# Performance work log

Measured on AMD Instinct MI355X. Metric: run time of the kernel, lower is better.

Reference implementation:

```python
import jax, jax.numpy as jnp
import numpy as np

H = 64
NUM_HEADS = 4
NUM_LAYERS = 2
B = 524288
EPS = 1e-5


def _layernorm(x, g, b):
    mu = jnp.mean(x, axis=-1, keepdims=True)
    var = jnp.mean((x - mu) ** 2, axis=-1, keepdims=True)
    return (x - mu) * jax.lax.rsqrt(var + EPS) * g + b


def _mha(x, w_qkv, b_qkv, w_o, b_o):
    # x: (B, M, H). Fused in-proj like torch nn.MultiheadAttention.
    Bx, M, Hx = x.shape
    hd = Hx // NUM_HEADS
    qkv = x @ w_qkv.T + b_qkv                      # (B, M, 3H)
    q, k, v = jnp.split(qkv, 3, axis=-1)
    q = q.reshape(Bx, M, NUM_HEADS, hd)
    k = k.reshape(Bx, M, NUM_HEADS, hd)
    v = v.reshape(Bx, M, NUM_HEADS, hd)
    scores = jnp.einsum('bqnd,bknd->bnqk', q, k) / jnp.sqrt(jnp.asarray(hd, x.dtype))
    a = jax.nn.softmax(scores, axis=-1)
    o = jnp.einsum('bnqk,bknd->bqnd', a, v).reshape(Bx, M, Hx)
    return o @ w_o.T + b_o


def _block(x, rel, p):
    attn_out = _mha(x, p['w_qkv'], p['b_qkv'], p['w_o'], p['b_o'])
    attn_out = attn_out * rel[:, :, None]
    x = _layernorm(x + attn_out, p['n1_g'], p['n1_b'])
    ffn = jax.nn.relu(x @ p['ffn_w'].T + p['ffn_b'])
    return _layernorm(x + ffn, p['n2_g'], p['n2_b'])


def setup_inputs() -> dict:
    key = jax.random.key(0)
    ks = jax.random.split(key, 32)
    inp = {
        'h_poi': jax.random.normal(ks[0], (B, H), jnp.float32),
        'h_census': jax.random.normal(ks[1], (B, H), jnp.float32),
        'h_traffic': jax.random.normal(ks[2], (B, H), jnp.float32),
        'mfr_poi': jax.random.uniform(ks[3], (B, 2), jnp.float32),
        'mfr_census': jax.random.uniform(ks[4], (B, 2), jnp.float32),
        'mfr_traffic': jax.random.uniform(ks[5], (B, 2), jnp.float32),
        'rel_w': jax.random.normal(ks[6], (1, 2), jnp.float32) * 0.5,
        'rel_b': jnp.zeros((1,), jnp.float32),
    }
    s = 1.0 / np.sqrt(H)
    for l in range(NUM_LAYERS):
        kk = jax.random.split(ks[7 + l], 6)
        inp[f'l{l}_w_qkv'] = jax.random.normal(kk[0], (3 * H, H), jnp.float32) * s
        inp[f'l{l}_b_qkv'] = jnp.zeros((3 * H,), jnp.float32)
        inp[f'l{l}_w_o'] = jax.random.normal(kk[1], (H, H), jnp.float32) * s
        inp[f'l{l}_b_o'] = jnp.zeros((H,), jnp.float32)
        inp[f'l{l}_ffn_w'] = jax.random.normal(kk[2], (H, H), jnp.float32) * s
        inp[f'l{l}_ffn_b'] = jnp.zeros((H,), jnp.float32)
        inp[f'l{l}_n1_g'] = jnp.ones((H,), jnp.float32)
        inp[f'l{l}_n1_b'] = jnp.zeros((H,), jnp.float32)
        inp[f'l{l}_n2_g'] = jnp.ones((H,), jnp.float32)
        inp[f'l{l}_n2_b'] = jnp.zeros((H,), jnp.float32)
    return inp


def reference(h_poi, h_census, h_traffic, mfr_poi, mfr_census, mfr_traffic,
              rel_w, rel_b,
              l0_w_qkv, l0_b_qkv, l0_w_o, l0_b_o, l0_ffn_w, l0_ffn_b,
              l0_n1_g, l0_n1_b, l0_n2_g, l0_n2_b,
              l1_w_qkv, l1_b_qkv, l1_w_o, l1_b_o, l1_ffn_w, l1_ffn_b,
              l1_n1_g, l1_n1_b, l1_n2_g, l1_n2_b):
    x = jnp.stack([h_poi, h_census, h_traffic], axis=1)  # (B, 3, H)
    rel = jax.nn.sigmoid(
        jnp.stack([mfr_poi, mfr_census, mfr_traffic], axis=1) @ rel_w.T + rel_b
    )[..., 0]                                            # (B, 3)
    layers = [
        dict(w_qkv=l0_w_qkv, b_qkv=l0_b_qkv, w_o=l0_w_o, b_o=l0_b_o,
             ffn_w=l0_ffn_w, ffn_b=l0_ffn_b, n1_g=l0_n1_g, n1_b=l0_n1_b,
             n2_g=l0_n2_g, n2_b=l0_n2_b),
        dict(w_qkv=l1_w_qkv, b_qkv=l1_b_qkv, w_o=l1_w_o, b_o=l1_b_o,
             ffn_w=l1_ffn_w, ffn_b=l1_ffn_b, n1_g=l1_n1_g, n1_b=l1_n1_b,
             n2_g=l1_n2_g, n2_b=l1_n2_b),
    ]
    for p in layers:
        x = _block(x, rel, p)
    return x  # (B, 3, H); slice [:, i, :] per modality if dict output desired
```

## Files before the change

### kernel.cpp

```cpp
#include <hip/hip_runtime.h>

typedef unsigned short u16;
typedef unsigned int u32;
typedef _Float16 h16;
typedef h16 h2v __attribute__((ext_vector_type(2)));
typedef h16 v8h __attribute__((ext_vector_type(8)));
typedef float v4f __attribute__((ext_vector_type(4)));

#define ROWS_PB 16
#define TOK 48
#define XS 76
#define QS 196
#define WS_L 20480

struct Params {
  const float *h0, *h1, *h2;
  const float *m0, *m1, *m2;
  const float *relw, *relb;
  const float *b_qkv[2], *b_o[2], *b_f[2];
  const float *n1g[2], *n1b[2], *n2g[2], *n2b[2];
  const u16* ws;
  float* out;
};

__device__ __forceinline__ u16 f2h(float f){ union{h16 h; u16 u;} c; c.h = (h16)f; return c.u; }
__device__ __forceinline__ float h2f(u16 u){ union{u16 u2; h16 h;} c; c.u2 = u; return (float)c.h; }

union Frag { uint2 u2[2]; uint4 u4; v8h v; };
union V16h { uint2 u2[4]; h2v h[8]; h16 s[16]; };

#if __has_builtin(__builtin_amdgcn_fdot2)
#define FDOT2(a,b,c) __builtin_amdgcn_fdot2((a),(b),(c),false)
#else
#define FDOT2(a,b,c) ((float)(a)[0]*(float)(b)[0] + (float)(a)[1]*(float)(b)[1] + (c))
#endif

__global__ __launch_bounds__(256, 2)
void prep_w(const float* wq0, const float* wo0, const float* wf0,
            const float* wq1, const float* wo1, const float* wf1, u16* ws){
  int idx = blockIdx.x * 256 + threadIdx.x;
  if (idx >= 2 * WS_L) return;
  int l = idx / WS_L, rem = idx % WS_L;
  const float* W; int loc;
  if (rem < 12288)      { W = l ? wq1 : wq0; loc = rem; }
  else if (rem < 16384) { W = l ? wo1 : wo0; loc = rem - 12288; }
  else                  { W = l ? wf1 : wf0; loc = rem - 16384; }
  int e = loc & 7, lane = (loc >> 3) & 63, fk = loc >> 9;
  int kk = fk & 1, nt = fk >> 1;
  int k = kk * 32 + 4 * (lane >> 4) + (e & 3) + (e >> 2) * 16;
  int n = nt * 16 + (lane & 15);
  ws[idx] = f2h(W[n * 64 + k]);
}

__device__ __forceinline__ v8h ldA(const u16* ap){
  Frag f;
  f.u2[0] = *(const uint2*)(ap);
  f.u2[1] = *(const uint2*)(ap + 16);
  return f.v;
}
__device__ __forceinline__ void ld16(V16h& o, const u16* p){
#pragma unroll
  for (int i = 0; i < 4; ++i) o.u2[i] = *(const uint2*)(p + 4 * i);
}

__device__ __forceinline__ float red16(float v){
  v += __shfl_xor(v, 1, 64);
  v += __shfl_xor(v, 2, 64);
  v += __shfl_xor(v, 4, 64);
  v += __shfl_xor(v, 8, 64);
  return v;
}

__global__ __launch_bounds__(192, 4)
void inter_encoder(Params p){
  __shared__ u16  sX[TOK * XS];
  __shared__ u16  sQKV[TOK * QS];
  __shared__ float sRel[TOK];

  const int tid  = threadIdx.x;
  const int lane = tid & 63, wv = tid >> 6;
  const int n15  = lane & 15, g = lane >> 4;
  const long long rowBase = (long long)blockIdx.x * ROWS_PB;

#pragma unroll
  for (int it = 0; it < 4; ++it){
    int idx = it * 192 + tid;
    int t = idx >> 4, c4 = (idx & 15) * 4;
    int r = t / 3, m = t - 3 * r;
    const float* hp = (m == 0) ? p.h0 : (m == 1) ? p.h1 : p.h2;
    float4 vv = *(const float4*)(hp + (rowBase + r) * 64 + c4);
    u32 lo = (u32)f2h(vv.x) | ((u32)f2h(vv.y) << 16);
    u32 hi = (u32)f2h(vv.z) | ((u32)f2h(vv.w) << 16);
    *(uint2*)(sX + t * XS + c4) = make_uint2(lo, hi);
  }
  if (tid < TOK){
    int t = tid, r = t / 3, m = t - 3 * r;
    const float* mf = (m == 0) ? p.m0 : (m == 1) ? p.m1 : p.m2;
    float a0 = mf[(rowBase + r) * 2 + 0], a1 = mf[(rowBase + r) * 2 + 1];
    float z = a0 * p.relw[0] + a1 * p.relw[1] + p.relb[0];
    sRel[t] = 1.f / (1.f + __expf(-z));
  }
  __syncthreads();

  for (int l = 0; l < 2; ++l){
    const u16* wsl = p.ws + l * WS_L;

    Frag aq[4][2];
    v4f bq4[4];
#pragma unroll
    for (int j = 0; j < 4; ++j){
      int mt = 4 * wv + j;
      aq[j][0].u4 = *(const uint4*)(wsl + ((mt * 2 + 0) * 64 + lane) * 8);
      aq[j][1].u4 = *(const uint4*)(wsl + ((mt * 2 + 1) * 64 + lane) * 8);
      bq4[j] = *(const v4f*)(p.b_qkv[l] + 16 * mt + 4 * g);
    }
#pragma unroll
    for (int nt = 0; nt < 3; ++nt){
      const u16* bp = sX + (16 * nt + n15) * XS + 4 * g;
      v8h b0 = ldA(bp), b1 = ldA(bp + 32);
#pragma unroll
      for (int j = 0; j < 4; ++j){
        v4f acc = bq4[j];
        acc = __builtin_amdgcn_mfma_f32_16x16x32_f16(aq[j][0].v, b0, acc, 0, 0, 0);
        acc = __builtin_amdgcn_mfma_f32_16x16x32_f16(aq[j][1].v, b1, acc, 0, 0, 0);
        u32 lo = (u32)f2h(acc[0]) | ((u32)f2h(acc[1]) << 16);
        u32 hi = (u32)f2h(acc[2]) | ((u32)f2h(acc[3]) << 16);
        *(uint2*)(sQKV + (16 * nt + n15) * QS + 16 * (4 * wv + j) + 4 * g)
            = make_uint2(lo, hi);
      }
    }
    __syncthreads();

    {
      const int t1 = wv, r = lane >> 2, h = lane & 3;
      const u16* base = sQKV + (3 * r) * QS + 16 * h;
      V16h q, k0, k1, k2;
      ld16(q,  base + t1 * QS);
      ld16(k0, base + 64);
      ld16(k1, base + QS + 64);
      ld16(k2, base + 2 * QS + 64);
      float s0 = 0.f, s1 = 0.f, s2 = 0.f;
#pragma unroll
      for (int pp = 0; pp < 8; ++pp){
        s0 = FDOT2(q.h[pp], k0.h[pp], s0);
        s1 = FDOT2(q.h[pp], k1.h[pp], s1);
        s2 = FDOT2(q.h[pp], k2.h[pp], s2);
      }
      s0 *= 0.25f; s1 *= 0.25f; s2 *= 0.25f;
      float mx = fmaxf(fmaxf(s0, s1), s2);
      float e0 = __expf(s0 - mx), e1 = __expf(s1 - mx), e2 = __expf(s2 - mx);
      float inv = 1.f / (e0 + e1 + e2);
      h16 w0 = (h16)(e0 * inv), w1 = (h16)(e1 * inv), w2 = (h16)(e2 * inv);
      h2v aw0 = {w0, w0}, aw1 = {w1, w1}, aw2 = {w2, w2};
      V16h v0, v1, v2, o;
      ld16(v0, base + 128);
      ld16(v1, base + QS + 128);
      ld16(v2, base + 2 * QS + 128);
#pragma unroll
      for (int pp = 0; pp < 8; ++pp)
        o.h[pp] = aw0 * v0.h[pp] + aw1 * v1.h[pp] + aw2 * v2.h[pp];
      u16* op = sQKV + (3 * r + t1) * QS + 16 * h;
#pragma unroll
      for (int pp = 0; pp < 4; ++pp) *(uint2*)(op + 4 * pp) = o.u2[pp];
    }
    __syncthreads();

    Frag bo[4][2];
    float biaso[4], g1v[4], b1v[4];
#pragma unroll
    for (int j = 0; j < 4; ++j){
#pragma unroll
      for (int kk = 0; kk < 2; ++kk)
        bo[j][kk].u4 = *(const uint4*)(wsl + 12288 + ((j * 2 + kk) * 64 + lane) * 8);
      biaso[j] = p.b_o[l][16 * j + n15];
      g1v[j] = p.n1g[l][16 * j + n15];
      b1v[j] = p.n1b[l][16 * j + n15];
    }
    {
      const u16* ap = sQKV + (16 * wv + n15) * QS + 4 * g;
      v8h a0 = ldA(ap), a1 = ldA(ap + 32);
      v4f acc[4];
#pragma unroll
      for (int j = 0; j < 4; ++j){
        acc[j] = (v4f){biaso[j], biaso[j], biaso[j], biaso[j]};
        acc[j] = __builtin_amdgcn_mfma_f32_16x16x32_f16(a0, bo[j][0].v, acc[j], 0, 0, 0);
        acc[j] = __builtin_amdgcn_mfma_f32_16x16x32_f16(a1, bo[j][1].v, acc[j], 0, 0, 0);
      }
#pragma unroll
      for (int i = 0; i < 4; ++i){
        int t = 16 * wv + 4 * g + i;
        float relt = sRel[t];
        float val[4], psum = 0.f;
#pragma unroll
        for (int j = 0; j < 4; ++j){
          val[j] = acc[j][i] * relt + h2f(sX[t * XS + 16 * j + n15]);
          psum += val[j];
        }
        float mu = red16(psum) * (1.f / 64.f);
        float dv[4], vs = 0.f;
#pragma unroll
        for (int j = 0; j < 4; ++j){ dv[j] = val[j] - mu; vs += dv[j] * dv[j]; }
        float rs = rsqrtf(red16(vs) * (1.f / 64.f) + 1e-5f);
#pragma unroll
        for (int j = 0; j < 4; ++j)
          sX[t * XS + 16 * j + n15] = f2h(dv[j] * rs * g1v[j] + b1v[j]);
      }
    }

    Frag bf[4][2];
    float biasf[4], g2v[4], b2v[4];
#pragma unroll
    for (int j = 0; j < 4; ++j){
#pragma unroll
      for (int kk = 0; kk < 2; ++kk)
        bf[j][kk].u4 = *(const uint4*)(wsl + 16384 + ((j * 2 + kk) * 64 + lane) * 8);
      biasf[j] = p.b_f[l][16 * j + n15];
      g2v[j] = p.n2g[l][16 * j + n15];
      b2v[j] = p.n2b[l][16 * j + n15];
    }
    {
      const u16* ap = sX + (16 * wv + n15) * XS + 4 * g;
      v8h a0 = ldA(ap), a1 = ldA(ap + 32);
      v4f acc[4];
#pragma unroll
      for (int j = 0; j < 4; ++j){
        acc[j] = (v4f){biasf[j], biasf[j], biasf[j], biasf[j]};
        acc[j] = __builtin_amdgcn_mfma_f32_16x16x32_f16(a0, bf[j][0].v, acc[j], 0, 0, 0);
        acc[j] = __builtin_amdgcn_mfma_f32_16x16x32_f16(a1, bf[j][1].v, acc[j], 0, 0, 0);
      }
#pragma unroll
      for (int i = 0; i < 4; ++i){
        int t = 16 * wv + 4 * g + i;
        float val[4], psum = 0.f;
#pragma unroll
        for (int j = 0; j < 4; ++j){
          val[j] = h2f(sX[t * XS + 16 * j + n15]) + fmaxf(acc[j][i], 0.f);
          psum += val[j];
        }
        float mu = red16(psum) * (1.f / 64.f);
        float dv[4], vs = 0.f;
#pragma unroll
        for (int j = 0; j < 4; ++j){ dv[j] = val[j] - mu; vs += dv[j] * dv[j]; }
        float rs = rsqrtf(red16(vs) * (1.f / 64.f) + 1e-5f);
#pragma unroll
        for (int j = 0; j < 4; ++j){
          float y = dv[j] * rs * g2v[j] + b2v[j];
          if (l == 0) sX[t * XS + 16 * j + n15] = f2h(y);
          else        p.out[(rowBase * 3 + t) * 64 + 16 * j + n15] = y;
        }
      }
    }
    __syncthreads();
  }
}

extern "C" void kernel_launch(void* const* d_in, const int* in_sizes, int n_in,
                              void* d_out, int out_size, void* d_ws, size_t ws_size,
                              hipStream_t stream){
  const float* const* in = (const float* const*)d_in;
  u16* ws = (u16*)d_ws;

  prep_w<<<(2 * WS_L + 255) / 256, 256, 0, stream>>>(
      in[8], in[10], in[12], in[18], in[20], in[22], ws);

  Params p;
  p.h0 = in[0]; p.h1 = in[1]; p.h2 = in[2];
  p.m0 = in[3]; p.m1 = in[4]; p.m2 = in[5];
  p.relw = in[6]; p.relb = in[7];
  for (int l = 0; l < 2; ++l){
    int b = 8 + 10 * l;
    p.b_qkv[l] = in[b + 1];
    p.b_o[l]   = in[b + 3];
    p.b_f[l]   = in[b + 5];
    p.n1g[l]   = in[b + 6]; p.n1b[l] = in[b + 7];
    p.n2g[l]   = in[b + 8]; p.n2b[l] = in[b + 9];
  }
  p.ws = ws;
  p.out = (float*)d_out;

  const int nblk = 524288 / ROWS_PB;
  inter_encoder<<<nblk, 192, 0, stream>>>(p);
}
```

Before: 464.9 us.

## Transpose out-proj and FFN MFMA so each lane owns a token row

Swaps the A/B operands of the output-projection and FFN MFMAs so the accumulator is transposed and each lane holds four contiguous features of one token. LayerNorm reductions become two cross-group shuffles instead of four-step 16-lane butterflies. Residual reads, LDS writes, parameter loads and the final global store are vectorised to 4-wide. It also drops the intermediate LDS round trip of the first LayerNorm output by keeping it in registers for the FFN residual. The cost is more live registers (val/y arrays), which may pressure the occupancy target.

```diff
diff --git a/kernel.cpp b/kernel.cpp
--- a/kernel.cpp
+++ b/kernel.cpp
@@ -24,10 +24,10 @@
 };
 
 __device__ __forceinline__ u16 f2h(float f){ union{h16 h; u16 u;} c; c.h = (h16)f; return c.u; }
-__device__ __forceinline__ float h2f(u16 u){ union{u16 u2; h16 h;} c; c.u2 = u; return (float)c.h; }
 
 union Frag { uint2 u2[2]; uint4 u4; v8h v; };
 union V16h { uint2 u2[4]; h2v h[8]; h16 s[16]; };
+union U2H  { uint2 u; h16 s[4]; };
 
 #if __has_builtin(__builtin_amdgcn_fdot2)
 #define FDOT2(a,b,c) __builtin_amdgcn_fdot2((a),(b),(c),false)
@@ -63,14 +63,6 @@
   for (int i = 0; i < 4; ++i) o.u2[i] = *(const uint2*)(p + 4 * i);
 }
 
-__device__ __forceinline__ float red16(float v){
-  v += __shfl_xor(v, 1, 64);
-  v += __shfl_xor(v, 2, 64);
-  v += __shfl_xor(v, 4, 64);
-  v += __shfl_xor(v, 8, 64);
-  return v;
-}
-
 __global__ __launch_bounds__(192, 4)
 void inter_encoder(Params p){
   __shared__ u16  sX[TOK * XS];
@@ -165,88 +157,107 @@
     }
     __syncthreads();
 
-    Frag bo[4][2];
-    float biaso[4], g1v[4], b1v[4];
-#pragma unroll
-    for (int j = 0; j < 4; ++j){
-#pragma unroll
-      for (int kk = 0; kk < 2; ++kk)
-        bo[j][kk].u4 = *(const uint4*)(wsl + 12288 + ((j * 2 + kk) * 64 + lane) * 8);
-      biaso[j] = p.b_o[l][16 * j + n15];
-      g1v[j] = p.n1g[l][16 * j + n15];
-      b1v[j] = p.n1b[l][16 * j + n15];
-    }
     {
-      const u16* ap = sQKV + (16 * wv + n15) * QS + 4 * g;
-      v8h a0 = ldA(ap), a1 = ldA(ap + 32);
-      v4f acc[4];
-#pragma unroll
-      for (int j = 0; j < 4; ++j){
-        acc[j] = (v4f){biaso[j], biaso[j], biaso[j], biaso[j]};
-        acc[j] = __builtin_amdgcn_mfma_f32_16x16x32_f16(a0, bo[j][0].v, acc[j], 0, 0, 0);
-        acc[j] = __builtin_amdgcn_mfma_f32_16x16x32_f16(a1, bo[j][1].v, acc[j], 0, 0, 0);
-      }
-#pragma unroll
-      for (int i = 0; i < 4; ++i){
-        int t = 16 * wv + 4 * g + i;
-        float relt = sRel[t];
-        float val[4], psum = 0.f;
+      const int trow = 16 * wv + n15;
+      const float relt = sRel[trow];
+      const u16* bp = sQKV + trow * QS + 4 * g;
+      v8h b0 = ldA(bp), b1 = ldA(bp + 32);
+
+      float val[4][4];
+      float psum = 0.f;
+#pragma unroll
+      for (int j = 0; j < 4; ++j){
+        Frag a0, a1;
+        a0.u4 = *(const uint4*)(wsl + 12288 + ((j * 2 + 0) * 64 + lane) * 8);
+        a1.u4 = *(const uint4*)(wsl + 12288 + ((j * 2 + 1) * 64 + lane) * 8);
+        v4f acc = *(const v4f*)(p.b_o[l] + 16 * j + 4 * g);
+        acc = __builtin_amdgcn_mfma_f32_16x16x32_f16(a0.v, b0, acc, 0, 0, 0);
+        acc = __builtin_amdgcn_mfma_f32_16x16x32_f16(a1.v, b1, acc, 0, 0, 0);
+        U2H x; x.u = *(const uint2*)(sX + trow * XS + 16 * j + 4 * g);
+#pragma unroll
+        for (int i = 0; i < 4; ++i){
+          val[j][i] = acc[i] * relt + (float)x.s[i];
+          psum += val[j][i];
+        }
+      }
+      psum += __shfl_xor(psum, 16, 64);
+      psum += __shfl_xor(psum, 32, 64);
+      float mu = psum * (1.f / 64.f);
+      float vs = 0.f;
+#pragma unroll
+      for (int j = 0; j < 4; ++j)
+#pragma unroll
+        for (int i = 0; i < 4; ++i){ float d = val[j][i] - mu; vs += d * d; }
+      vs += __shfl_xor(vs, 16, 64);
+      vs += __shfl_xor(vs, 32, 64);
+      float rs = rsqrtf(vs * (1.f / 64.f) + 1e-5f);
+
+      float y[4][4];
+#pragma unroll
+      for (int j = 0; j < 4; ++j){
+        v4f gg = *(const v4f*)(p.n1g[l] + 16 * j + 4 * g);
+        v4f bb = *(const v4f*)(p.n1b[l] + 16 * j + 4 * g);
+#pragma unroll
+        for (int i = 0; i < 4; ++i) y[j][i] = (val[j][i] - mu) * rs * gg[i] + bb[i];
+        u32 lo = (u32)f2h(y[j][0]) | ((u32)f2h(y[j][1]) << 16);
+        u32 hi = (u32)f2h(y[j][2]) | ((u32)f2h(y[j][3]) << 16);
+        *(uint2*)(sX + trow * XS + 16 * j + 4 * g) = make_uint2(lo, hi);
+      }
+
+      const u16* ap2 = sX + trow * XS + 4 * g;
+      v8h c0 = ldA(ap2), c1 = ldA(ap2 + 32);
+
+      float psum2 = 0.f;
+#pragma unroll
+      for (int j = 0; j < 4; ++j){
+        Frag a0, a1;
+        a0.u4 = *(const uint4*)(wsl + 16384 + ((j * 2 + 0) * 64 + lane) * 8);
+        a1.u4 = *(const uint4*)(wsl + 16384 + ((j * 2 + 1) * 64 + lane) * 8);
+        v4f acc = *(const v4f*)(p.b_f[l] + 16 * j + 4 * g);
+        acc = __builtin_amdgcn_mfma_f32_16x16x32_f16(a0.v, c0, acc, 0, 0, 0);
+        acc = __builtin_amdgcn_mfma_f32_16x16x32_f16(a1.v, c1, acc, 0, 0, 0);
+#pragma unroll
+        for (int i = 0; i < 4; ++i){
+          float v2 = y[j][i] + fmaxf(acc[i], 0.f);
+          val[j][i] = v2;
+          psum2 += v2;
+        }
+      }
+      psum2 += __shfl_xor(psum2, 16, 64);
+      psum2 += __shfl_xor(psum2, 32, 64);
+      float mu2 = psum2 * (1.f / 64.f);
+      float vs2 = 0.f;
+#pragma unroll
+      for (int j = 0; j < 4; ++j)
+#pragma unroll
+        for (int i = 0; i < 4; ++i){ float d = val[j][i] - mu2; vs2 += d * d; }
+      vs2 += __shfl_xor(vs2, 16, 64);
+      vs2 += __shfl_xor(vs2, 32, 64);
+      float rs2 = rsqrtf(vs2 * (1.f / 64.f) + 1e-5f);
+
+      if (l == 0){
 #pragma unroll
         for (int j = 0; j < 4; ++j){
-          val[j] = acc[j][i] * relt + h2f(sX[t * XS + 16 * j + n15]);
-          psum += val[j];
-        }
-        float mu = red16(psum) * (1.f / 64.f);
-        float dv[4], vs = 0.f;
-#pragma unroll
-        for (int j = 0; j < 4; ++j){ dv[j] = val[j] - mu; vs += dv[j] * dv[j]; }
-        float rs = rsqrtf(red16(vs) * (1.f / 64.f) + 1e-5f);
-#pragma unroll
-        for (int j = 0; j < 4; ++j)
-          sX[t * XS + 16 * j + n15] = f2h(dv[j] * rs * g1v[j] + b1v[j]);
-      }
-    }
-
-    Frag bf[4][2];
-    float biasf[4], g2v[4], b2v[4];
-#pragma unroll
-    for (int j = 0; j < 4; ++j){
-#pragma unroll
-      for (int kk = 0; kk < 2; ++kk)
-        bf[j][kk].u4 = *(const uint4*)(wsl + 16384 + ((j * 2 + kk) * 64 + lane) * 8);
-      biasf[j] = p.b_f[l][16 * j + n15];
-      g2v[j] = p.n2g[l][16 * j + n15];
-      b2v[j] = p.n2b[l][16 * j + n15];
-    }
-    {
-      const u16* ap = sX + (16 * wv + n15) * XS + 4 * g;
-      v8h a0 = ldA(ap), a1 = ldA(ap + 32);
-      v4f acc[4];
-#pragma unroll
-      for (int j = 0; j < 4; ++j){
-        acc[j] = (v4f){biasf[j], biasf[j], biasf[j], biasf[j]};
-        acc[j] = __builtin_amdgcn_mfma_f32_16x16x32_f16(a0, bf[j][0].v, acc[j], 0, 0, 0);
-        acc[j] = __builtin_amdgcn_mfma_f32_16x16x32_f16(a1, bf[j][1].v, acc[j], 0, 0, 0);
-      }
-#pragma unroll
-      for (int i = 0; i < 4; ++i){
-        int t = 16 * wv + 4 * g + i;
-        float val[4], psum = 0.f;
+          v4f gg = *(const v4f*)(p.n2g[0] + 16 * j + 4 * g);
+          v4f bb = *(const v4f*)(p.n2b[0] + 16 * j + 4 * g);
+          float z0 = (val[j][0] - mu2) * rs2 * gg[0] + bb[0];
+          float z1 = (val[j][1] - mu2) * rs2 * gg[1] + bb[1];
+          float z2 = (val[j][2] - mu2) * rs2 * gg[2] + bb[2];
+          float z3 = (val[j][3] - mu2) * rs2 * gg[3] + bb[3];
+          u32 lo = (u32)f2h(z0) | ((u32)f2h(z1) << 16);
+          u32 hi = (u32)f2h(z2) | ((u32)f2h(z3) << 16);
+          *(uint2*)(sX + trow * XS + 16 * j + 4 * g) = make_uint2(lo, hi);
+        }
+      } else {
+        float* op = p.out + (rowBase * 3 + trow) * 64;
 #pragma unroll
         for (int j = 0; j < 4; ++j){
-          val[j] = h2f(sX[t * XS + 16 * j + n15]) + fmaxf(acc[j][i], 0.f);
-          psum += val[j];
-        }
-        float mu = red16(psum) * (1.f / 64.f);
-        float dv[4], vs = 0.f;
-#pragma unroll
-        for (int j = 0; j < 4; ++j){ dv[j] = val[j] - mu; vs += dv[j] * dv[j]; }
-        float rs = rsqrtf(red16(vs) * (1.f / 64.f) + 1e-5f);
-#pragma unroll
-        for (int j = 0; j < 4; ++j){
-          float y = dv[j] * rs * g2v[j] + b2v[j];
-          if (l == 0) sX[t * XS + 16 * j + n15] = f2h(y);
-          else        p.out[(rowBase * 3 + t) * 64 + 16 * j + n15] = y;
+          v4f gg = *(const v4f*)(p.n2g[1] + 16 * j + 4 * g);
+          v4f bb = *(const v4f*)(p.n2b[1] + 16 * j + 4 * g);
+          v4f yo;
+#pragma unroll
+          for (int i = 0; i < 4; ++i) yo[i] = (val[j][i] - mu2) * rs2 * gg[i] + bb[i];
+          *(v4f*)(op + 16 * j + 4 * g) = yo;
         }
       }
     }
```

Result: faster. 444.5 us (-4.4%).
